# Kernel tuning notes

Measured on AMD Instinct MI355X. Metric: run time of the kernel, lower is better.

## Reference

```python
import itertools
import jax, jax.numpy as jnp
import numpy as np

ORDER = 3  # MaskDE(order=3) -> DescartesExtension orders 2..3
D = 80
B = 8192


def setup_inputs() -> dict:
    key = jax.random.key(0)
    kx, km = jax.random.split(key)
    x = jax.random.normal(kx, (B, D), dtype=jnp.float32)
    mask = jax.random.randint(km, (D,), 0, 2).astype(jnp.bool_)
    return {"x": x, "mask": mask}


def _comb_indices(m: int, order: int) -> np.ndarray:
    # combinations with replacement of range(m), shape (n_comb, order)
    return np.array(list(itertools.combinations_with_replacement(range(m), order)), dtype=np.int32)


def reference(x, mask):
    # mask is a concrete bool vector: masked_select == static gather
    idx = np.flatnonzero(np.asarray(mask))  # (m,)
    m = idx.size
    xm = x[:, idx]  # (B, m)
    parts = [xm]
    for order in range(2, ORDER + 1):
        combs = _comb_indices(m, order)           # (C, order)
        # gather-multiply-reduce: prod of each feature combination
        parts.append(jnp.prod(xm[:, combs], axis=-1))  # (B, C)
    return jnp.concatenate(parts, axis=-1)
```

## Files before the change

kernel.cpp:

```cpp
#include <hip/hip_runtime.h>
#include <stdint.h>

#define DMAX 80
#define BLK  256
#define XW   96
#define EPB  4096

typedef float f32x4 __attribute__((ext_vector_type(4)));

__global__ void maskde_setup(const void* __restrict__ mask_raw, int m,
                             int* __restrict__ idx_out,
                             uint32_t* __restrict__ coltab,
                             int tpad, int T, int P) {
    int tid = blockIdx.x * blockDim.x + threadIdx.x;

    if (tid == 0) {
        const uint8_t* b8  = (const uint8_t*)mask_raw;
        const int*     b32 = (const int*)mask_raw;
        const float*   bf  = (const float*)mask_raw;
        int cnt = 0; bool ok = true;
        for (int i = 0; i < DMAX; ++i) { uint8_t v = b8[i]; if (v > 1) ok = false; cnt += (v != 0); }
        int mode;
        if (ok && cnt == m) {
            mode = 0;
        } else {
            cnt = 0; ok = true;
            for (int i = 0; i < DMAX; ++i) { int v = b32[i]; if (v != 0 && v != 1) ok = false; cnt += (v != 0); }
            mode = (ok && cnt == m) ? 1 : 2;
        }
        int k = 0;
        for (int i = 0; i < DMAX && k < m; ++i) {
            bool on = (mode == 0) ? (b8[i] != 0)
                    : (mode == 1) ? (b32[i] != 0)
                                  : (bf[i] != 0.0f);
            if (on) idx_out[k++] = i;
        }
    }

    int stride = gridDim.x * blockDim.x;
    for (int p = tid; p < P; p += stride) {
        int rem = p, i = 0;
        while (rem >= m - i) { rem -= (m - i); ++i; }
        int j = i + rem;

        #define WR4(c, v) do {                                              \
            int _c = (c); uint32_t _v = (v);                                \
            coltab[_c] = _v;                                                \
            if (_c >= 1) coltab[tpad     + _c - 1] = _v;                    \
            if (_c >= 2) coltab[2 * tpad + _c - 2] = _v;                    \
            if (_c >= 3) coltab[3 * tpad + _c - 3] = _v;                    \
        } while (0)

        uint32_t mm8  = (uint32_t)m << 8;
        uint32_t mm16 = (uint32_t)m << 16;
        if (p < m)
            WR4(p, (uint32_t)p | mm8 | mm16);
        WR4(m + p, (uint32_t)i | ((uint32_t)j << 8) | mm16);

        int mi = m - i;
        long long Si  = ((long long)m * (m + 1) * (m + 2)
                       - (long long)mi * (mi + 1) * (mi + 2)) / 6;
        int Rij = ((m - i) + (m - j + 1)) * (j - i) / 2;
        int base = m + P + (int)Si + Rij;
        uint32_t ij = (uint32_t)i | ((uint32_t)j << 8);
        for (int k3 = j; k3 < m; ++k3)
            WR4(base + (k3 - j), ij | ((uint32_t)k3 << 16));
        #undef WR4
    }
}

__global__ void maskde_xsel(const float* __restrict__ x,
                            const int* __restrict__ idx,
                            float* __restrict__ xsel, int m, int rows) {
    int g = blockIdx.x * BLK + threadIdx.x;
    int total = rows * XW;
    for (; g < total; g += gridDim.x * BLK) {
        int row = g / XW, k = g - row * XW;
        xsel[g] = (k < m) ? x[row * DMAX + idx[k]] : 1.0f;
    }
}

__global__ __launch_bounds__(BLK) void
maskde_expand(const float* __restrict__ xsel,
              const uint32_t* __restrict__ coltab, int tpad,
              float* __restrict__ out, int T, int rows, int total) {
    __shared__ float xls0[XW];
    __shared__ float xls1[XW];

    const int tid  = threadIdx.x;
    const int e0   = blockIdx.x * EPB;
    if (e0 >= total) return;
    const int eend = (e0 + EPB < total) ? e0 + EPB : total;
    const int r0   = e0 / T;
    const int r0start = r0 * T;
    const bool need1 = ((eend - 1) / T) > r0;

    if (tid < XW) {
        xls0[tid] = xsel[r0 * XW + tid];
    } else if (tid >= 128 && tid < 128 + XW) {
        int k = tid - 128;
        xls1[k] = need1 ? xsel[(r0 + 1) * XW + k] : 1.0f;
    }
    __syncthreads();

#pragma unroll
    for (int it = 0; it < EPB / (4 * BLK); ++it) {
        int ee = e0 + (tid << 2) + it * (4 * BLK);
        if (ee >= total) break;
        int c = ee - r0start;
        const float* xS = xls0;
        if (c >= T) { c -= T; xS = xls1; }

        if (c <= T - 4 && ee + 3 < total) {
            int s = c & 3;
            uint4 t = *(const uint4*)(coltab + (size_t)s * tpad + (c - s));
            f32x4 o;
            o.x = xS[t.x & 0xFF] * xS[(t.x >> 8) & 0xFF] * xS[t.x >> 16];
            o.y = xS[t.y & 0xFF] * xS[(t.y >> 8) & 0xFF] * xS[t.y >> 16];
            o.z = xS[t.z & 0xFF] * xS[(t.z >> 8) & 0xFF] * xS[t.z >> 16];
            o.w = xS[t.w & 0xFF] * xS[(t.w >> 8) & 0xFF] * xS[t.w >> 16];
            *(f32x4*)(out + ee) = o;
        } else {
            for (int u = 0; u < 4; ++u) {
                int e2 = ee + u;
                if (e2 >= total) break;
                int c2 = e2 - r0start;
                const float* x2 = xls0;
                if (c2 >= T) { c2 -= T; x2 = xls1; }
                uint32_t en = coltab[c2];
                out[e2] = x2[en & 0xFF] * x2[(en >> 8) & 0xFF] * x2[en >> 16];
            }
        }
    }
}

extern "C" void kernel_launch(void* const* d_in, const int* in_sizes, int n_in,
                              void* d_out, int out_size, void* d_ws, size_t ws_size,
                              hipStream_t stream) {
    const float* x    = (const float*)d_in[0];
    const void*  mask = d_in[1];
    float*       out  = (float*)d_out;

    int rows = in_sizes[0] / DMAX;
    if (rows <= 0 || out_size <= 0) return;
    long long Tll = (long long)out_size / rows;

    int m = -1;
    for (int mm = 0; mm <= DMAX; ++mm) {
        long long t = (long long)mm
                    + (long long)mm * (mm + 1) / 2
                    + (long long)mm * (mm + 1) * (mm + 2) / 6;
        if (t == Tll) { m = mm; break; }
    }
    if (m <= 0) return;

    int T     = (int)Tll;
    int P     = m * (m + 1) / 2;
    int tpad  = (T + 3) & ~3;
    int total = rows * T;

    char* ws = (char*)d_ws;
    int*      idx    = (int*)ws;
    uint32_t* coltab = (uint32_t*)(ws + 32768);
    size_t off_xsel  = 32768 + (size_t)4 * tpad * 4 + 256;
    off_xsel = (off_xsel + 255) & ~(size_t)255;
    float*    xsel   = (float*)(ws + off_xsel);

    int sblocks = (P + 255) / 256;
    if (sblocks < 1) sblocks = 1;
    maskde_setup<<<sblocks, 256, 0, stream>>>(mask, m, idx, coltab,
                                              tpad, T, P);

    int xblocks = (rows * XW + BLK - 1) / BLK;
    if (xblocks > 2048) xblocks = 2048;
    maskde_xsel<<<xblocks, BLK, 0, stream>>>(x, idx, xsel, m, rows);

    int nb = (total + EPB - 1) / EPB;
    maskde_expand<<<nb, BLK, 0, stream>>>(xsel, coltab, tpad,
                                          out, T, rows, total);
}
```

Baseline: 123.9 us.

## Tile expand kernel over row groups and column chunks, reusing coltab loads

The expand kernel now uses a 2D grid of row groups by 1024-column chunks instead of flat 4096-element spans. Each block stages four rows spaced four apart, which share the same 16-byte output alignment, and reuses each uint4 coltab load for all four rows. Unaligned head and tail elements are handled by a few scalar threads. This cuts per-element index math, row-boundary branching and redundant coltab traffic, at the cost of more complex indexing and some idle threads in the partial last chunk.

```diff
diff --git a/kernel.cpp b/kernel.cpp
--- a/kernel.cpp
+++ b/kernel.cpp
@@ -4,7 +4,8 @@
 #define DMAX 80
 #define BLK  256
 #define XW   96
-#define EPB  4096
+#define CW   1024
+#define R    4
 
 typedef float f32x4 __attribute__((ext_vector_type(4)));
 
@@ -83,52 +84,80 @@
 __global__ __launch_bounds__(BLK) void
 maskde_expand(const float* __restrict__ xsel,
               const uint32_t* __restrict__ coltab, int tpad,
-              float* __restrict__ out, int T, int rows, int total) {
-    __shared__ float xls0[XW];
-    __shared__ float xls1[XW];
-
-    const int tid  = threadIdx.x;
-    const int e0   = blockIdx.x * EPB;
-    if (e0 >= total) return;
-    const int eend = (e0 + EPB < total) ? e0 + EPB : total;
-    const int r0   = e0 / T;
-    const int r0start = r0 * T;
-    const bool need1 = ((eend - 1) / T) > r0;
-
-    if (tid < XW) {
-        xls0[tid] = xsel[r0 * XW + tid];
-    } else if (tid >= 128 && tid < 128 + XW) {
-        int k = tid - 128;
-        xls1[k] = need1 ? xsel[(r0 + 1) * XW + k] : 1.0f;
+              float* __restrict__ out, int T, int rows,
+              int ncc, int gpc) {
+    __shared__ float xls[R][XW];
+
+    const int tid = threadIdx.x;
+    const int rg  = blockIdx.x / ncc;
+    const int cc  = blockIdx.x - rg * ncc;
+    const int cls = rg / gpc;
+    const int gix = rg - cls * gpc;
+
+    const int row0 = cls + 16 * gix;
+    const int c0   = cc * CW;
+    const int cend = (c0 + CW < T) ? c0 + CW : T;
+
+    for (int q = tid; q < R * XW; q += BLK) {
+        int u = q / XW, k = q - u * XW;
+        int row = row0 + 4 * u;
+        xls[u][k] = (row < rows) ? xsel[row * XW + k] : 1.0f;
     }
     __syncthreads();
 
+    const long long rs0 = (long long)row0 * T;
+    const int a4 = (int)((rs0 + c0) & 3);
+    const int d  = (4 - a4) & 3;
+    int cd = c0 + d;
+    if (cd > cend) cd = cend;
+    const int nq   = (cend - cd) >> 2;
+    const int ct   = cd + 4 * nq;
+    const int tcnt = cend - ct;
+
+    const int s = cd & 3;
+    const uint4* tb = (const uint4*)(coltab + (size_t)s * tpad + (cd & ~3));
+
+    float* ob[R];
+    int nr = 0;
 #pragma unroll
-    for (int it = 0; it < EPB / (4 * BLK); ++it) {
-        int ee = e0 + (tid << 2) + it * (4 * BLK);
-        if (ee >= total) break;
-        int c = ee - r0start;
-        const float* xS = xls0;
-        if (c >= T) { c -= T; xS = xls1; }
-
-        if (c <= T - 4 && ee + 3 < total) {
-            int s = c & 3;
-            uint4 t = *(const uint4*)(coltab + (size_t)s * tpad + (c - s));
-            f32x4 o;
-            o.x = xS[t.x & 0xFF] * xS[(t.x >> 8) & 0xFF] * xS[t.x >> 16];
-            o.y = xS[t.y & 0xFF] * xS[(t.y >> 8) & 0xFF] * xS[t.y >> 16];
-            o.z = xS[t.z & 0xFF] * xS[(t.z >> 8) & 0xFF] * xS[t.z >> 16];
-            o.w = xS[t.w & 0xFF] * xS[(t.w >> 8) & 0xFF] * xS[t.w >> 16];
-            *(f32x4*)(out + ee) = o;
-        } else {
-            for (int u = 0; u < 4; ++u) {
-                int e2 = ee + u;
-                if (e2 >= total) break;
-                int c2 = e2 - r0start;
-                const float* x2 = xls0;
-                if (c2 >= T) { c2 -= T; x2 = xls1; }
-                uint32_t en = coltab[c2];
-                out[e2] = x2[en & 0xFF] * x2[(en >> 8) & 0xFF] * x2[en >> 16];
+    for (int u = 0; u < R; ++u) {
+        int row = row0 + 4 * u;
+        if (row < rows) { ob[u] = out + (size_t)row * T + cd; nr = u + 1; }
+        else            { ob[u] = nullptr; }
+    }
+
+    if (tid < 8) {
+        int u = tid >> 1, half = tid & 1;
+        if (u < nr && ob[u]) {
+            if (half == 0) {
+                for (int w = 0; w < d; ++w) {
+                    uint32_t e = coltab[c0 + w];
+                    ob[u][w - d] = xls[u][e & 0xFF] * xls[u][(e >> 8) & 0xFF]
+                                 * xls[u][e >> 16];
+                }
+            } else {
+                for (int w = 0; w < tcnt; ++w) {
+                    uint32_t e = coltab[ct + w];
+                    ob[u][(ct - cd) + w] = xls[u][e & 0xFF]
+                                         * xls[u][(e >> 8) & 0xFF]
+                                         * xls[u][e >> 16];
+                }
+            }
+        }
+    }
+
+    for (int q = tid; q < nq; q += BLK) {
+        uint4 t = tb[q];
+#pragma unroll
+        for (int u = 0; u < R; ++u) {
+            if (ob[u]) {
+                const float* xr = xls[u];
+                f32x4 o;
+                o.x = xr[t.x & 0xFF] * xr[(t.x >> 8) & 0xFF] * xr[t.x >> 16];
+                o.y = xr[t.y & 0xFF] * xr[(t.y >> 8) & 0xFF] * xr[t.y >> 16];
+                o.z = xr[t.z & 0xFF] * xr[(t.z >> 8) & 0xFF] * xr[t.z >> 16];
+                o.w = xr[t.w & 0xFF] * xr[(t.w >> 8) & 0xFF] * xr[t.w >> 16];
+                *(f32x4*)(ob[u] + 4 * q) = o;
             }
         }
     }
@@ -154,10 +183,9 @@
     }
     if (m <= 0) return;
 
-    int T     = (int)Tll;
-    int P     = m * (m + 1) / 2;
-    int tpad  = (T + 3) & ~3;
-    int total = rows * T;
+    int T    = (int)Tll;
+    int P    = m * (m + 1) / 2;
+    int tpad = (T + 3) & ~3;
 
     char* ws = (char*)d_ws;
     int*      idx    = (int*)ws;
@@ -175,7 +203,10 @@
     if (xblocks > 2048) xblocks = 2048;
     maskde_xsel<<<xblocks, BLK, 0, stream>>>(x, idx, xsel, m, rows);
 
-    int nb = (total + EPB - 1) / EPB;
-    maskde_expand<<<nb, BLK, 0, stream>>>(xsel, coltab, tpad,
-                                          out, T, rows, total);
-}
+    int ncc = (T + CW - 1) / CW;
+    int rpc = (rows + 3) / 4;
+    int gpc = (rpc + R - 1) / R;
+    int nb  = 4 * gpc * ncc;
+    maskde_expand<<<nb, BLK, 0, stream>>>(xsel, coltab, tpad, out,
+                                          T, rows, ncc, gpc);
+}
```

Result: slower. 161.5 us (+30.3%).

## Make expand kernel persistent with double-buffered prefetch of selected rows

Applied to the files above, without the earlier changes.

The expand kernel now launches a fixed grid of up to 2048 blocks that loop over output chunks instead of one block per chunk. While computing a chunk, each block prefetches the next chunk's selected-feature rows into registers and then stores them into a second shared-memory buffer. This aims to hide the global load latency at chunk start and cut block launch overhead. In exchange it adds a barrier per chunk and may reduce the scheduler's load balancing on a store-bound kernel.

```diff
diff --git a/kernel.cpp b/kernel.cpp
--- a/kernel.cpp
+++ b/kernel.cpp
@@ -1,10 +1,11 @@
 #include <hip/hip_runtime.h>
 #include <stdint.h>
 
-#define DMAX 80
-#define BLK  256
-#define XW   96
-#define EPB  4096
+#define DMAX  80
+#define BLK   256
+#define XW    96
+#define EPB   4096
+#define PGRID 2048
 
 typedef float f32x4 __attribute__((ext_vector_type(4)));
 
@@ -83,53 +84,75 @@
 __global__ __launch_bounds__(BLK) void
 maskde_expand(const float* __restrict__ xsel,
               const uint32_t* __restrict__ coltab, int tpad,
-              float* __restrict__ out, int T, int rows, int total) {
-    __shared__ float xls0[XW];
-    __shared__ float xls1[XW];
-
-    const int tid  = threadIdx.x;
-    const int e0   = blockIdx.x * EPB;
-    if (e0 >= total) return;
-    const int eend = (e0 + EPB < total) ? e0 + EPB : total;
-    const int r0   = e0 / T;
-    const int r0start = r0 * T;
-    const bool need1 = ((eend - 1) / T) > r0;
-
-    if (tid < XW) {
-        xls0[tid] = xsel[r0 * XW + tid];
-    } else if (tid >= 128 && tid < 128 + XW) {
-        int k = tid - 128;
-        xls1[k] = need1 ? xsel[(r0 + 1) * XW + k] : 1.0f;
+              float* __restrict__ out, int T, int rows, int total,
+              int nchunks) {
+    __shared__ float xls[2][2][XW];
+
+    const int tid = threadIdx.x;
+    const int gslot = (tid < XW) ? 0 : ((tid >= 128 && tid < 128 + XW) ? 1 : -1);
+    const int gk    = (gslot == 1) ? tid - 128 : tid;
+
+    int ch = blockIdx.x;
+    if (ch >= nchunks) return;
+
+    if (gslot >= 0) {
+        int r0  = (ch * EPB) / T;
+        int row = r0 + gslot;
+        xls[0][gslot][gk] = (row < rows) ? xsel[row * XW + gk] : 1.0f;
     }
     __syncthreads();
 
+    int cur = 0;
+    for (; ch < nchunks; ch += PGRID) {
+        const int e0      = ch * EPB;
+        const int r0      = e0 / T;
+        const int r0start = r0 * T;
+
+        const int nch = ch + PGRID;
+        float pf = 1.0f;
+        if (nch < nchunks && gslot >= 0) {
+            int nr = (nch * EPB) / T + gslot;
+            if (nr < rows) pf = xsel[nr * XW + gk];
+        }
+
+        const float* xls0 = xls[cur][0];
+        const float* xls1 = xls[cur][1];
+
 #pragma unroll
-    for (int it = 0; it < EPB / (4 * BLK); ++it) {
-        int ee = e0 + (tid << 2) + it * (4 * BLK);
-        if (ee >= total) break;
-        int c = ee - r0start;
-        const float* xS = xls0;
-        if (c >= T) { c -= T; xS = xls1; }
-
-        if (c <= T - 4 && ee + 3 < total) {
-            int s = c & 3;
-            uint4 t = *(const uint4*)(coltab + (size_t)s * tpad + (c - s));
-            f32x4 o;
-            o.x = xS[t.x & 0xFF] * xS[(t.x >> 8) & 0xFF] * xS[t.x >> 16];
-            o.y = xS[t.y & 0xFF] * xS[(t.y >> 8) & 0xFF] * xS[t.y >> 16];
-            o.z = xS[t.z & 0xFF] * xS[(t.z >> 8) & 0xFF] * xS[t.z >> 16];
-            o.w = xS[t.w & 0xFF] * xS[(t.w >> 8) & 0xFF] * xS[t.w >> 16];
-            *(f32x4*)(out + ee) = o;
-        } else {
-            for (int u = 0; u < 4; ++u) {
-                int e2 = ee + u;
-                if (e2 >= total) break;
-                int c2 = e2 - r0start;
-                const float* x2 = xls0;
-                if (c2 >= T) { c2 -= T; x2 = xls1; }
-                uint32_t en = coltab[c2];
-                out[e2] = x2[en & 0xFF] * x2[(en >> 8) & 0xFF] * x2[en >> 16];
+        for (int it = 0; it < EPB / (4 * BLK); ++it) {
+            int ee = e0 + (tid << 2) + it * (4 * BLK);
+            if (ee >= total) break;
+            int c = ee - r0start;
+            const float* xS = xls0;
+            if (c >= T) { c -= T; xS = xls1; }
+
+            if (c <= T - 4 && ee + 3 < total) {
+                int s = c & 3;
+                uint4 t = *(const uint4*)(coltab + (size_t)s * tpad + (c - s));
+                f32x4 o;
+                o.x = xS[t.x & 0xFF] * xS[(t.x >> 8) & 0xFF] * xS[t.x >> 16];
+                o.y = xS[t.y & 0xFF] * xS[(t.y >> 8) & 0xFF] * xS[t.y >> 16];
+                o.z = xS[t.z & 0xFF] * xS[(t.z >> 8) & 0xFF] * xS[t.z >> 16];
+                o.w = xS[t.w & 0xFF] * xS[(t.w >> 8) & 0xFF] * xS[t.w >> 16];
+                *(f32x4*)(out + ee) = o;
+            } else {
+                for (int u = 0; u < 4; ++u) {
+                    int e2 = ee + u;
+                    if (e2 >= total) break;
+                    int c2 = e2 - r0start;
+                    const float* x2 = xls0;
+                    if (c2 >= T) { c2 -= T; x2 = xls1; }
+                    uint32_t en = coltab[c2];
+                    out[e2] = x2[en & 0xFF] * x2[(en >> 8) & 0xFF]
+                            * x2[en >> 16];
+                }
             }
+        }
+
+        if (nch < nchunks) {
+            if (gslot >= 0) xls[cur ^ 1][gslot][gk] = pf;
+            __syncthreads();
+            cur ^= 1;
         }
     }
 }
@@ -154,10 +177,11 @@
     }
     if (m <= 0) return;
 
-    int T     = (int)Tll;
-    int P     = m * (m + 1) / 2;
-    int tpad  = (T + 3) & ~3;
-    int total = rows * T;
+    int T       = (int)Tll;
+    int P       = m * (m + 1) / 2;
+    int tpad    = (T + 3) & ~3;
+    int total   = rows * T;
+    int nchunks = (total + EPB - 1) / EPB;
 
     char* ws = (char*)d_ws;
     int*      idx    = (int*)ws;
@@ -175,7 +199,7 @@
     if (xblocks > 2048) xblocks = 2048;
     maskde_xsel<<<xblocks, BLK, 0, stream>>>(x, idx, xsel, m, rows);
 
-    int nb = (total + EPB - 1) / EPB;
-    maskde_expand<<<nb, BLK, 0, stream>>>(xsel, coltab, tpad,
-                                          out, T, rows, total);
-}
+    int pg = (nchunks < PGRID) ? nchunks : PGRID;
+    maskde_expand<<<pg, BLK, 0, stream>>>(xsel, coltab, tpad, out,
+                                          T, rows, total, nchunks);
+}
```

Result: slower. 132.3 us (+6.7%).
